# Performance work log

Hardware: AMD Instinct MI355X
Metric: run time of the kernel (lower is better)

## Reference

```python
import jax, jax.numpy as jnp
import numpy as np
from jax import lax

PATCH = 11          # patch_size
DIL = 2             # dilation_patch
PAD = (PATCH // 2) * DIL  # 10
EPS = 1e-5


def setup_inputs() -> dict:
    key = jax.random.key(0)
    k0, k1, kw, kb, kg, kbe = jax.random.split(key, 6)
    B, C, H, W = 8, 128, 192, 192
    x0 = jax.random.normal(k0, (B, C, H, W), dtype=jnp.float32)
    x1 = jax.random.normal(k1, (B, C, H, W), dtype=jnp.float32)
    # Conv2d(121, 8, k=3, s=1, p=1) params + BatchNorm2d(8) affine params
    conv_w = jax.random.normal(kw, (8, 121, 3, 3), dtype=jnp.float32) * 0.05
    conv_b = jax.random.normal(kb, (8,), dtype=jnp.float32) * 0.05
    gamma = jnp.ones((8,), dtype=jnp.float32)
    beta = jnp.zeros((8,), dtype=jnp.float32)
    return {"x0": x0, "x1": x1, "conv_w": conv_w, "conv_b": conv_b,
            "gamma": gamma, "beta": beta}


def _correlation(x0, x1):
    """spatial_correlation_sample(kernel=1, patch=11, stride=1, pad=0, dil_patch=2).
    out[b, pi*11+pj, i, j] = sum_c x0[b,c,i,j] * x1[b,c, i+(pi-5)*2, j+(pj-5)*2]
    (zero-padded outside)."""
    x1p = jnp.pad(x1, ((0, 0), (0, 0), (PAD, PAD), (PAD, PAD)))
    slices = []
    for pi in range(PATCH):       # static 11x11 displacement grid
        for pj in range(PATCH):
            x1s = lax.dynamic_slice(x1p, (0, 0, pi * DIL, pj * DIL), x1.shape)
            slices.append(jnp.einsum('bchw,bchw->bhw', x0, x1s))
    return jnp.stack(slices, axis=1)  # [B, 121, H, W]


def reference(x0, x1, conv_w, conv_b, gamma, beta):
    y = _correlation(x0, x1)  # [B, 121, H, W]
    y = lax.conv_general_dilated(y, conv_w, window_strides=(1, 1),
                                 padding=((1, 1), (1, 1)),
                                 dimension_numbers=('NCHW', 'OIHW', 'NCHW'))
    y = y + conv_b[None, :, None, None]
    # BatchNorm2d in training mode: batch statistics over (B, H, W), biased var
    mean = jnp.mean(y, axis=(0, 2, 3))
    var = jnp.var(y, axis=(0, 2, 3))
    y = (y - mean[None, :, None, None]) * (gamma / jnp.sqrt(var + EPS))[None, :, None, None] \
        + beta[None, :, None, None]
    return jax.nn.relu(y)
```

## Files before the change

kernel.cpp:

```cpp
#include <hip/hip_runtime.h>

#define HH 192
#define WW 192
#define CC 128
#define BB 8
#define HW (HH * WW)
#define OC 8
#define NPIX (BB * HW)
#define YCHUNK (OC * BB * HW)
#define X0ROW 24576
#define X1ROW 28672

typedef __attribute__((ext_vector_type(8))) short bf16x8;
typedef __attribute__((ext_vector_type(4))) float f32x4;

__device__ __forceinline__ unsigned short f2bf(float f) {
    unsigned int u = __float_as_uint(f);
    u += 0x7fffu + ((u >> 16) & 1u);
    return (unsigned short)(u >> 16);
}
__device__ __forceinline__ float bf2f(unsigned short u) {
    return __uint_as_float(((unsigned int)u) << 16);
}

__global__ __launch_bounds__(256) void k_pack(
    const float* __restrict__ x0, const float* __restrict__ x1,
    unsigned short* __restrict__ x0t, unsigned short* __restrict__ x1t)
{
    const int h = blockIdx.x, b = blockIdx.y, t = blockIdx.z;
    const float* src = t ? x1 : x0;
    __shared__ unsigned short lds[WW * 130];

    for (int idx = threadIdx.x; idx < CC * WW; idx += 256) {
        const int w = idx % WW, c = idx / WW;
        lds[w * 130 + c] = f2bf(src[((size_t)(b * CC + c) * HH + h) * WW + w]);
    }
    __syncthreads();

    if (t == 0) {
        unsigned int* dst = (unsigned int*)(x0t + (size_t)(b * HH + h) * X0ROW);
        for (int f2 = threadIdx.x; f2 < X0ROW / 2; f2 += 256) {
            const int e2  = f2 & 3;
            const int pxl = (f2 >> 2) & 15;
            const int kg  = (f2 >> 6) & 3;
            const int q   = (f2 >> 8) & 3;
            const int pu  = f2 >> 10;
            const int ut  = pu % 6, par = pu / 6;
            const int px  = 2 * (16 * ut + pxl) + par;
            const int c   = q * 32 + kg * 8 + e2 * 2;
            const unsigned int lo = lds[px * 130 + c];
            const unsigned int hi = lds[px * 130 + c + 1];
            dst[f2] = lo | (hi << 16);
        }
    } else {
        unsigned int* dst = (unsigned int*)(x1t + (size_t)(b * HH + h) * X1ROW);
        for (int f2 = threadIdx.x; f2 < X1ROW / 2; f2 += 256) {
            const int e2  = f2 & 3;
            const int pxl = (f2 >> 2) & 15;
            const int kg  = (f2 >> 6) & 3;
            const int q   = (f2 >> 8) & 3;
            const int pv  = f2 >> 10;
            const int vt  = pv % 7, par = pv / 7;
            const int v   = 16 * vt - 8 + pxl;
            unsigned int val = 0;
            if (v >= 0 && v < 96) {
                const int px = 2 * v + par;
                const int c  = q * 32 + kg * 8 + e2 * 2;
                val = lds[px * 130 + c] | ((unsigned int)lds[px * 130 + c + 1] << 16);
            }
            dst[f2] = val;
        }
    }
}

__global__ __launch_bounds__(384, 8) void k_corr_mfma_conv(
    const unsigned short* __restrict__ x0t, const unsigned short* __restrict__ x1t,
    const float* __restrict__ cw, const float* __restrict__ cb,
    float* __restrict__ y0, float* __restrict__ y1, float* __restrict__ y2)
{
    const int L = blockIdx.x;
    const int w = (L & 7) * 96 + (L >> 3);
    const int b     = w / 96;
    const int rem   = w % 96;
    const int part  = rem >> 5;
    const int strip = rem & 31;
    const int i0    = strip * 6;
    const int plo   = (11 * part) / 3;
    const int phi   = (11 * (part + 1)) / 3;

    const int tid  = threadIdx.x;
    const int wave = tid >> 6, lane = tid & 63;
    const int ln15 = lane & 15, kg = lane >> 4;
    const int u0   = wave * 16;

    __shared__ unsigned short corr[8][194][11];

    if (tid < 176) {
        const int ir = tid / 22, rr = tid % 22;
        const int pj = rr % 11, jj = (rr < 11) ? 0 : 193;
        corr[ir][jj][pj] = 0;
    }

    float yacc[3][OC];
#pragma unroll
    for (int k = 0; k < 3; ++k)
#pragma unroll
        for (int o = 0; o < OC; ++o) yacc[k][o] = 0.f;

    const int jt  = tid % 192;
    const int irb = tid / 192;

    const unsigned short* x0b = x0t + (size_t)b * HH * X0ROW;
    const unsigned short* x1b = x1t + (size_t)b * HH * X1ROW;

    for (int pi = plo; pi < phi; ++pi) {
        __syncthreads();

        for (int ir = 0; ir < 8; ++ir) {
            const int i = i0 - 1 + ir;
            const int r = i + 2 * pi - 10;
            const bool gv = (i >= 0) && (i < HH) && (r >= 0) && (r < HH);
            const int icl = min(max(i, 0), HH - 1);
            const int rcl = min(max(r, 0), HH - 1);
            const unsigned short* arow = x0b + (size_t)icl * X0ROW + lane * 8;
            const unsigned short* brow = x1b + (size_t)rcl * X1ROW + lane * 8;

#pragma unroll
            for (int par = 0; par < 2; ++par) {
                const unsigned short* pa = arow + (par * 6 + wave) * 2048;
                const bf16x8 a0 = *(const bf16x8*)(pa);
                const bf16x8 a1 = *(const bf16x8*)(pa + 512);
                const bf16x8 a2 = *(const bf16x8*)(pa + 1024);
                const bf16x8 a3 = *(const bf16x8*)(pa + 1536);

#pragma unroll
                for (int vtl = 0; vtl < 2; ++vtl) {
                    const unsigned short* pb =
                        brow + (par * 7 + wave + vtl) * 2048;
                    const bf16x8 b0 = *(const bf16x8*)(pb);
                    const bf16x8 b1 = *(const bf16x8*)(pb + 512);
                    const bf16x8 b2 = *(const bf16x8*)(pb + 1024);
                    const bf16x8 b3 = *(const bf16x8*)(pb + 1536);

                    f32x4 c = {0.f, 0.f, 0.f, 0.f};
                    c = __builtin_amdgcn_mfma_f32_16x16x32_bf16(a0, b0, c, 0, 0, 0);
                    c = __builtin_amdgcn_mfma_f32_16x16x32_bf16(a1, b1, c, 0, 0, 0);
                    c = __builtin_amdgcn_mfma_f32_16x16x32_bf16(a2, b2, c, 0, 0, 0);
                    c = __builtin_amdgcn_mfma_f32_16x16x32_bf16(a3, b3, c, 0, 0, 0);

                    const int v = u0 - 8 + 16 * vtl + ln15;
#pragma unroll
                    for (int rg = 0; rg < 4; ++rg) {
                        const int u  = u0 + kg * 4 + rg;
                        const int pj = v - u + 5;
                        if (pj >= 0 && pj < 11)
                            corr[ir][2 * u + par + 1][pj] = f2bf(gv ? c[rg] : 0.f);
                    }
                }
            }
        }
        __syncthreads();

        for (int ki = 0; ki < 3; ++ki) {
            for (int kj = 0; kj < 3; ++kj) {
                float cv[3][11];
#pragma unroll
                for (int k = 0; k < 3; ++k) {
                    const unsigned short* cp = &corr[irb + 2 * k + ki][jt + kj][0];
#pragma unroll
                    for (int pj = 0; pj < 11; ++pj) cv[k][pj] = bf2f(cp[pj]);
                }
#pragma unroll
                for (int o = 0; o < OC; ++o) {
                    float a0 = yacc[0][o], a1 = yacc[1][o], a2 = yacc[2][o];
#pragma unroll
                    for (int pj = 0; pj < 11; ++pj) {
                        const float wv =
                            cw[o * 1089 + (pi * 11 + pj) * 9 + ki * 3 + kj];
                        a0 = fmaf(wv, cv[0][pj], a0);
                        a1 = fmaf(wv, cv[1][pj], a1);
                        a2 = fmaf(wv, cv[2][pj], a2);
                    }
                    yacc[0][o] = a0; yacc[1][o] = a1; yacc[2][o] = a2;
                }
            }
        }
    }

    float* yp = (part == 0) ? y0 : ((part == 1) ? y1 : y2);
#pragma unroll
    for (int k = 0; k < 3; ++k) {
        const int irow = i0 + irb + 2 * k;
#pragma unroll
        for (int o = 0; o < OC; ++o) {
            float val = yacc[k][o];
            if (part == 0) val += cb[o];
            yp[((size_t)(b * OC + o) * HH + irow) * WW + jt] = val;
        }
    }
}

__global__ __launch_bounds__(256) void k_corr_conv(
    const float* __restrict__ x0, const float* __restrict__ x1,
    const float* __restrict__ cw, const float* __restrict__ cb,
    float* __restrict__ y)
{
    const int b  = blockIdx.z;
    const int i0 = blockIdx.y * 14;
    const int j0 = blockIdx.x * 14;
    const int li = threadIdx.x >> 4;
    const int lj = threadIdx.x & 15;
    const int gi = i0 + li - 1;
    const int gj = j0 + lj - 1;
    const bool valid    = (gi >= 0) & (gi < HH) & (gj >= 0) & (gj < WW);
    const bool interior = (li >= 1) & (li <= 14) & (lj >= 1) & (lj <= 14)
                        & (gi < HH) & (gj < WW);

    __shared__ float corr[16][16][13];

    float yacc[OC];
#pragma unroll
    for (int o = 0; o < OC; ++o) yacc[o] = 0.f;

    const size_t bbase = (size_t)b * CC * HW;
    const float* x0p = x0 + bbase + (size_t)gi * WW + gj;

    for (int pi = 0; pi < 11; ++pi) {
        float acc[11];
#pragma unroll
        for (int k = 0; k < 11; ++k) acc[k] = 0.f;

        const int r = gi + 2 * pi - 10;
        if (valid && r >= 0 && r < HH) {
            const float* p0 = x0p;
            if (gj >= 10 && gj <= WW - 11) {
                const float* p1o = x1 + bbase + (size_t)r * WW + (gj - 10);
#pragma unroll 2
                for (int c = 0; c < CC; ++c) {
                    const float a = *p0;
#pragma unroll
                    for (int k = 0; k < 11; ++k)
                        acc[k] = fmaf(a, p1o[2 * k], acc[k]);
                    p0 += HW; p1o += HW;
                }
            } else {
                const float* p1 = x1 + bbase + (size_t)r * WW;
#pragma unroll 2
                for (int c = 0; c < CC; ++c) {
                    const float a = *p0;
#pragma unroll
                    for (int k = 0; k < 11; ++k) {
                        const int col = gj + 2 * k - 10;
                        const float v = (col >= 0 && col < WW) ? p1[col] : 0.f;
                        acc[k] = fmaf(a, v, acc[k]);
                    }
                    p0 += HW; p1 += HW;
                }
            }
        }

        __syncthreads();
#pragma unroll
        for (int k = 0; k < 11; ++k) corr[li][lj][k] = acc[k];
        __syncthreads();

        if (interior) {
#pragma unroll
            for (int ki = 0; ki < 3; ++ki) {
#pragma unroll
                for (int kj = 0; kj < 3; ++kj) {
                    float cv[11];
#pragma unroll
                    for (int k = 0; k < 11; ++k)
                        cv[k] = corr[li + ki - 1][lj + kj - 1][k];
#pragma unroll
                    for (int o = 0; o < OC; ++o) {
#pragma unroll
                        for (int k = 0; k < 11; ++k) {
                            const float wv =
                                cw[(((o * 121) + pi * 11 + k) * 3 + ki) * 3 + kj];
                            yacc[o] = fmaf(wv, cv[k], yacc[o]);
                        }
                    }
                }
            }
        }
    }

    if (interior) {
#pragma unroll
        for (int o = 0; o < OC; ++o)
            y[(size_t)(b * OC + o) * HW + (size_t)gi * WW + gj] = yacc[o] + cb[o];
    }
}

__global__ __launch_bounds__(256) void k_stats_partial(
    const float* __restrict__ y0, const float* __restrict__ y1,
    const float* __restrict__ y2, int n, float* __restrict__ st)
{
    const int bid = blockIdx.x;
    const int b = bid >> 5, rem = bid & 31;
    const int o = rem >> 2, q = rem & 3;
    const size_t off = (size_t)(b * OC + o) * (HW / 4) + q * (HW / 16);
    const float4* p0 = (const float4*)y0 + off;
    const float4* p1 = (const float4*)y1 + off;
    const float4* p2 = (const float4*)y2 + off;
    float s = 0.f, qq = 0.f;
    for (int t = threadIdx.x; t < HW / 16; t += 256) {
        float4 z = p0[t];
        if (n >= 2) {
            const float4 v = p1[t];
            z.x += v.x; z.y += v.y; z.z += v.z; z.w += v.w;
        }
        if (n >= 3) {
            const float4 v = p2[t];
            z.x += v.x; z.y += v.y; z.z += v.z; z.w += v.w;
        }
        s += z.x + z.y + z.z + z.w;
        qq = fmaf(z.x, z.x, qq); qq = fmaf(z.y, z.y, qq);
        qq = fmaf(z.z, z.z, qq); qq = fmaf(z.w, z.w, qq);
    }
#pragma unroll
    for (int off2 = 32; off2 > 0; off2 >>= 1) {
        s  += __shfl_down(s, off2);
        qq += __shfl_down(qq, off2);
    }
    __shared__ float ss[4], sq[4];
    const int lane = threadIdx.x & 63, wv = threadIdx.x >> 6;
    if (lane == 0) { ss[wv] = s; sq[wv] = qq; }
    __syncthreads();
    if (threadIdx.x == 0) {
        st[bid]       = ss[0] + ss[1] + ss[2] + ss[3];
        st[256 + bid] = sq[0] + sq[1] + sq[2] + sq[3];
    }
}

__global__ void k_stats_final(float* __restrict__ st,
                              const float* __restrict__ gamma,
                              const float* __restrict__ beta)
{
    const int o = threadIdx.x;
    if (o < 8) {
        float S = 0.f, Q = 0.f;
#pragma unroll
        for (int b = 0; b < 8; ++b)
#pragma unroll
            for (int q = 0; q < 4; ++q) {
                S += st[b * 32 + o * 4 + q];
                Q += st[256 + b * 32 + o * 4 + q];
            }
        const float invN = 1.f / (float)NPIX;
        const float mean = S * invN;
        const float var  = Q * invN - mean * mean;
        const float sc   = gamma[o] / sqrtf(var + 1e-5f);
        st[512 + o] = sc;
        st[520 + o] = beta[o] - mean * sc;
    }
}

__global__ __launch_bounds__(256) void k_bn_relu(
    const float* __restrict__ y0, const float* __restrict__ y1,
    const float* __restrict__ y2, int n,
    const float* __restrict__ st, float* __restrict__ out)
{
    const int i = blockIdx.x * 256 + threadIdx.x;
    const int o = (i / (HW / 4)) & 7;
    const float sc = st[512 + o], sh = st[520 + o];
    float4 z = ((const float4*)y0)[i];
    if (n >= 2) {
        const float4 v = ((const float4*)y1)[i];
        z.x += v.x; z.y += v.y; z.z += v.z; z.w += v.w;
    }
    if (n >= 3) {
        const float4 v = ((const float4*)y2)[i];
        z.x += v.x; z.y += v.y; z.z += v.z; z.w += v.w;
    }
    float4 r;
    r.x = fmaxf(fmaf(z.x, sc, sh), 0.f);
    r.y = fmaxf(fmaf(z.y, sc, sh), 0.f);
    r.z = fmaxf(fmaf(z.z, sc, sh), 0.f);
    r.w = fmaxf(fmaf(z.w, sc, sh), 0.f);
    ((float4*)out)[i] = r;
}

extern "C" void kernel_launch(void* const* d_in, const int* in_sizes, int n_in,
                              void* d_out, int out_size, void* d_ws, size_t ws_size,
                              hipStream_t stream)
{
    const float* x0    = (const float*)d_in[0];
    const float* x1    = (const float*)d_in[1];
    const float* cw    = (const float*)d_in[2];
    const float* cb    = (const float*)d_in[3];
    const float* gamma = (const float*)d_in[4];
    const float* beta  = (const float*)d_in[5];
    float* out = (float*)d_out;
    float* st  = (float*)d_ws;

    const size_t x0bytes = (size_t)BB * HH * X0ROW * sizeof(unsigned short);
    const size_t x1bytes = (size_t)BB * HH * X1ROW * sizeof(unsigned short);
    const size_t ybytes  = (size_t)YCHUNK * sizeof(float);

    if (ws_size >= x0bytes + x1bytes + 2 * ybytes) {
        unsigned short* x0t = (unsigned short*)d_ws;
        unsigned short* x1t = (unsigned short*)((char*)d_ws + x0bytes);
        float* y1           = (float*)((char*)d_ws + x0bytes + x1bytes);
        float* y2           = (float*)((char*)d_ws + x0bytes + x1bytes + ybytes);

        k_pack<<<dim3(HH, BB, 2), 256, 0, stream>>>(x0, x1, x0t, x1t);
        k_corr_mfma_conv<<<768, 384, 0, stream>>>(x0t, x1t, cw, cb, out, y1, y2);
        k_stats_partial<<<256, 256, 0, stream>>>(out, y1, y2, 3, st);
        k_stats_final<<<1, 64, 0, stream>>>(st, gamma, beta);
        k_bn_relu<<<(YCHUNK / 4) / 256, 256, 0, stream>>>(out, y1, y2, 3, st, out);
    } else {
        dim3 g1(14, 14, 8);
        k_corr_conv<<<g1, 256, 0, stream>>>(x0, x1, cw, cb, out);
        k_stats_partial<<<256, 256, 0, stream>>>(out, out, out, 1, st);
        k_stats_final<<<1, 64, 0, stream>>>(st, gamma, beta);
        k_bn_relu<<<(YCHUNK / 4) / 256, 256, 0, stream>>>(out, out, out, 1, st, out);
    }
}
```

Baseline: 530.9 us.

## Process two pi displacement rows per sync and split work into two parts

The correlation+conv kernel now splits the 11 vertical displacements across 2 parts instead of 3, giving 512 blocks instead of 768. Within each block it computes two pi rows per iteration into a double-sized LDS correlation buffer. This reuses the x0 fragment loads across both displacements and halves the number of barriers. It also drops one partial-output buffer and the stats/BN pass over it. In exchange, LDS use and register pressure rise, occupancy falls (the launch-bounds min-blocks hint is removed), and fewer blocks may underfill the GPU.

Result: slower. 554.7 us (+4.5%).

```diff
diff --git a/kernel.cpp b/kernel.cpp
--- a/kernel.cpp
+++ b/kernel.cpp
@@ -73,32 +73,33 @@
     }
 }
 
-__global__ __launch_bounds__(384, 8) void k_corr_mfma_conv(
+__global__ __launch_bounds__(384) void k_corr_mfma_conv(
     const unsigned short* __restrict__ x0t, const unsigned short* __restrict__ x1t,
     const float* __restrict__ cw, const float* __restrict__ cb,
-    float* __restrict__ y0, float* __restrict__ y1, float* __restrict__ y2)
+    float* __restrict__ y0, float* __restrict__ y1)
 {
     const int L = blockIdx.x;
-    const int w = (L & 7) * 96 + (L >> 3);
-    const int b     = w / 96;
-    const int rem   = w % 96;
+    const int w = (L & 7) * 64 + (L >> 3);
+    const int b     = w >> 6;
+    const int rem   = w & 63;
     const int part  = rem >> 5;
     const int strip = rem & 31;
     const int i0    = strip * 6;
-    const int plo   = (11 * part) / 3;
-    const int phi   = (11 * (part + 1)) / 3;
+    const int plo   = part ? 6 : 0;
+    const int phi   = part ? 11 : 6;
 
     const int tid  = threadIdx.x;
     const int wave = tid >> 6, lane = tid & 63;
     const int ln15 = lane & 15, kg = lane >> 4;
     const int u0   = wave * 16;
 
-    __shared__ unsigned short corr[8][194][11];
-
-    if (tid < 176) {
-        const int ir = tid / 22, rr = tid % 22;
+    __shared__ unsigned short corr[2][8][194][11];
+
+    if (tid < 352) {
+        const int sl = tid / 176, r2 = tid % 176;
+        const int ir = r2 / 22, rr = r2 % 22;
         const int pj = rr % 11, jj = (rr < 11) ? 0 : 193;
-        corr[ir][jj][pj] = 0;
+        corr[sl][ir][jj][pj] = 0;
     }
 
     float yacc[3][OC];
@@ -113,17 +114,15 @@
     const unsigned short* x0b = x0t + (size_t)b * HH * X0ROW;
     const unsigned short* x1b = x1t + (size_t)b * HH * X1ROW;
 
-    for (int pi = plo; pi < phi; ++pi) {
+    for (int p0 = plo; p0 < phi; p0 += 2) {
+        const int npair = (p0 + 1 < phi) ? 2 : 1;
         __syncthreads();
 
         for (int ir = 0; ir < 8; ++ir) {
-            const int i = i0 - 1 + ir;
-            const int r = i + 2 * pi - 10;
-            const bool gv = (i >= 0) && (i < HH) && (r >= 0) && (r < HH);
+            const int i   = i0 - 1 + ir;
+            const bool iv = (i >= 0) && (i < HH);
             const int icl = min(max(i, 0), HH - 1);
-            const int rcl = min(max(r, 0), HH - 1);
             const unsigned short* arow = x0b + (size_t)icl * X0ROW + lane * 8;
-            const unsigned short* brow = x1b + (size_t)rcl * X1ROW + lane * 8;
 
 #pragma unroll
             for (int par = 0; par < 2; ++par) {
@@ -134,60 +133,80 @@
                 const bf16x8 a3 = *(const bf16x8*)(pa + 1536);
 
 #pragma unroll
-                for (int vtl = 0; vtl < 2; ++vtl) {
-                    const unsigned short* pb =
-                        brow + (par * 7 + wave + vtl) * 2048;
-                    const bf16x8 b0 = *(const bf16x8*)(pb);
-                    const bf16x8 b1 = *(const bf16x8*)(pb + 512);
-                    const bf16x8 b2 = *(const bf16x8*)(pb + 1024);
-                    const bf16x8 b3 = *(const bf16x8*)(pb + 1536);
-
-                    f32x4 c = {0.f, 0.f, 0.f, 0.f};
-                    c = __builtin_amdgcn_mfma_f32_16x16x32_bf16(a0, b0, c, 0, 0, 0);
-                    c = __builtin_amdgcn_mfma_f32_16x16x32_bf16(a1, b1, c, 0, 0, 0);
-                    c = __builtin_amdgcn_mfma_f32_16x16x32_bf16(a2, b2, c, 0, 0, 0);
-                    c = __builtin_amdgcn_mfma_f32_16x16x32_bf16(a3, b3, c, 0, 0, 0);
-
-                    const int v = u0 - 8 + 16 * vtl + ln15;
-#pragma unroll
-                    for (int rg = 0; rg < 4; ++rg) {
-                        const int u  = u0 + kg * 4 + rg;
-                        const int pj = v - u + 5;
-                        if (pj >= 0 && pj < 11)
-                            corr[ir][2 * u + par + 1][pj] = f2bf(gv ? c[rg] : 0.f);
+                for (int p2 = 0; p2 < 2; ++p2) {
+                    if (p2 < npair) {
+                        const int pi = p0 + p2;
+                        const int r  = i + 2 * pi - 10;
+                        const bool gv = iv && (r >= 0) && (r < HH);
+                        const int rcl = min(max(r, 0), HH - 1);
+                        const unsigned short* brow =
+                            x1b + (size_t)rcl * X1ROW + lane * 8;
+
+#pragma unroll
+                        for (int vtl = 0; vtl < 2; ++vtl) {
+                            const unsigned short* pb =
+                                brow + (par * 7 + wave + vtl) * 2048;
+                            const bf16x8 b0 = *(const bf16x8*)(pb);
+                            const bf16x8 b1 = *(const bf16x8*)(pb + 512);
+                            const bf16x8 b2 = *(const bf16x8*)(pb + 1024);
+                            const bf16x8 b3 = *(const bf16x8*)(pb + 1536);
+
+                            f32x4 c = {0.f, 0.f, 0.f, 0.f};
+                            c = __builtin_amdgcn_mfma_f32_16x16x32_bf16(a0, b0, c, 0, 0, 0);
+                            c = __builtin_amdgcn_mfma_f32_16x16x32_bf16(a1, b1, c, 0, 0, 0);
+                            c = __builtin_amdgcn_mfma_f32_16x16x32_bf16(a2, b2, c, 0, 0, 0);
+                            c = __builtin_amdgcn_mfma_f32_16x16x32_bf16(a3, b3, c, 0, 0, 0);
+
+                            const int v = u0 - 8 + 16 * vtl + ln15;
+#pragma unroll
+                            for (int rg = 0; rg < 4; ++rg) {
+                                const int u  = u0 + kg * 4 + rg;
+                                const int pj = v - u + 5;
+                                if (pj >= 0 && pj < 11)
+                                    corr[p2][ir][2 * u + par + 1][pj] =
+                                        f2bf(gv ? c[rg] : 0.f);
+                            }
+                        }
                     }
                 }
             }
         }
         __syncthreads();
 
-        for (int ki = 0; ki < 3; ++ki) {
-            for (int kj = 0; kj < 3; ++kj) {
-                float cv[3][11];
-#pragma unroll
-                for (int k = 0; k < 3; ++k) {
-                    const unsigned short* cp = &corr[irb + 2 * k + ki][jt + kj][0];
-#pragma unroll
-                    for (int pj = 0; pj < 11; ++pj) cv[k][pj] = bf2f(cp[pj]);
+#pragma unroll
+        for (int p2 = 0; p2 < 2; ++p2) {
+            if (p2 < npair) {
+                const int pi = p0 + p2;
+                for (int ki = 0; ki < 3; ++ki) {
+                    for (int kj = 0; kj < 3; ++kj) {
+                        float cv[3][11];
+#pragma unroll
+                        for (int k = 0; k < 3; ++k) {
+                            const unsigned short* cp =
+                                &corr[p2][irb + 2 * k + ki][jt + kj][0];
+#pragma unroll
+                            for (int pj = 0; pj < 11; ++pj) cv[k][pj] = bf2f(cp[pj]);
+                        }
+#pragma unroll
+                        for (int o = 0; o < OC; ++o) {
+                            float a0 = yacc[0][o], a1 = yacc[1][o], a2 = yacc[2][o];
+#pragma unroll
+                            for (int pj = 0; pj < 11; ++pj) {
+                                const float wv =
+                                    cw[o * 1089 + (pi * 11 + pj) * 9 + ki * 3 + kj];
+                                a0 = fmaf(wv, cv[0][pj], a0);
+                                a1 = fmaf(wv, cv[1][pj], a1);
+                                a2 = fmaf(wv, cv[2][pj], a2);
+                            }
+                            yacc[0][o] = a0; yacc[1][o] = a1; yacc[2][o] = a2;
+                        }
+                    }
                 }
-#pragma unroll
-                for (int o = 0; o < OC; ++o) {
-                    float a0 = yacc[0][o], a1 = yacc[1][o], a2 = yacc[2][o];
-#pragma unroll
-                    for (int pj = 0; pj < 11; ++pj) {
-                        const float wv =
-                            cw[o * 1089 + (pi * 11 + pj) * 9 + ki * 3 + kj];
-                        a0 = fmaf(wv, cv[0][pj], a0);
-                        a1 = fmaf(wv, cv[1][pj], a1);
-                        a2 = fmaf(wv, cv[2][pj], a2);
-                    }
-                    yacc[0][o] = a0; yacc[1][o] = a1; yacc[2][o] = a2;
-                }
-            }
-        }
-    }
-
-    float* yp = (part == 0) ? y0 : ((part == 1) ? y1 : y2);
+            }
+        }
+    }
+
+    float* yp = part ? y1 : y0;
 #pragma unroll
     for (int k = 0; k < 3; ++k) {
         const int irow = i0 + irb + 2 * k;
@@ -400,17 +419,16 @@
     const size_t x1bytes = (size_t)BB * HH * X1ROW * sizeof(unsigned short);
     const size_t ybytes  = (size_t)YCHUNK * sizeof(float);
 
-    if (ws_size >= x0bytes + x1bytes + 2 * ybytes) {
+    if (ws_size >= x0bytes + x1bytes + ybytes) {
         unsigned short* x0t = (unsigned short*)d_ws;
         unsigned short* x1t = (unsigned short*)((char*)d_ws + x0bytes);
         float* y1           = (float*)((char*)d_ws + x0bytes + x1bytes);
-        float* y2           = (float*)((char*)d_ws + x0bytes + x1bytes + ybytes);
 
         k_pack<<<dim3(HH, BB, 2), 256, 0, stream>>>(x0, x1, x0t, x1t);
-        k_corr_mfma_conv<<<768, 384, 0, stream>>>(x0t, x1t, cw, cb, out, y1, y2);
-        k_stats_partial<<<256, 256, 0, stream>>>(out, y1, y2, 3, st);
+        k_corr_mfma_conv<<<512, 384, 0, stream>>>(x0t, x1t, cw, cb, out, y1);
+        k_stats_partial<<<256, 256, 0, stream>>>(out, y1, y1, 2, st);
         k_stats_final<<<1, 64, 0, stream>>>(st, gamma, beta);
-        k_bn_relu<<<(YCHUNK / 4) / 256, 256, 0, stream>>>(out, y1, y2, 3, st, out);
+        k_bn_relu<<<(YCHUNK / 4) / 256, 256, 0, stream>>>(out, y1, y1, 2, st, out);
     } else {
         dim3 g1(14, 14, 8);
         k_corr_conv<<<g1, 256, 0, stream>>>(x0, x1, cw, cb, out);
```

## Double-buffer MFMA operand loads in correlation loop and vectorize pack stores

Applied to the files above, without the earlier changes.

The correlation phase now software-pipelines its global loads: operands for the next (row, parity) step are loaded into a second register set while MFMAs run on the current one, so memory latency can hide behind compute. Launch bounds drop from 8 to 4 waves-per-EU minimum to give the extra register buffers room, at the cost of occupancy. The pack kernel also writes 16-byte vectors instead of 4-byte words.

After: 795.9 us. 49.9% more time.

```diff
diff --git a/kernel.cpp b/kernel.cpp
--- a/kernel.cpp
+++ b/kernel.cpp
@@ -38,42 +38,95 @@
     __syncthreads();
 
     if (t == 0) {
-        unsigned int* dst = (unsigned int*)(x0t + (size_t)(b * HH + h) * X0ROW);
-        for (int f2 = threadIdx.x; f2 < X0ROW / 2; f2 += 256) {
-            const int e2  = f2 & 3;
-            const int pxl = (f2 >> 2) & 15;
-            const int kg  = (f2 >> 6) & 3;
-            const int q   = (f2 >> 8) & 3;
-            const int pu  = f2 >> 10;
+        uint4* dst = (uint4*)(x0t + (size_t)(b * HH + h) * X0ROW);
+        for (int f8 = threadIdx.x; f8 < X0ROW / 8; f8 += 256) {
+            const int pxl = f8 & 15;
+            const int kg  = (f8 >> 4) & 3;
+            const int q   = (f8 >> 6) & 3;
+            const int pu  = f8 >> 8;
             const int ut  = pu % 6, par = pu / 6;
             const int px  = 2 * (16 * ut + pxl) + par;
-            const int c   = q * 32 + kg * 8 + e2 * 2;
-            const unsigned int lo = lds[px * 130 + c];
-            const unsigned int hi = lds[px * 130 + c + 1];
-            dst[f2] = lo | (hi << 16);
+            const unsigned short* s0 = &lds[px * 130 + q * 32 + kg * 8];
+            uint4 v;
+            v.x = s0[0] | ((unsigned int)s0[1] << 16);
+            v.y = s0[2] | ((unsigned int)s0[3] << 16);
+            v.z = s0[4] | ((unsigned int)s0[5] << 16);
+            v.w = s0[6] | ((unsigned int)s0[7] << 16);
+            dst[f8] = v;
         }
     } else {
-        unsigned int* dst = (unsigned int*)(x1t + (size_t)(b * HH + h) * X1ROW);
-        for (int f2 = threadIdx.x; f2 < X1ROW / 2; f2 += 256) {
-            const int e2  = f2 & 3;
-            const int pxl = (f2 >> 2) & 15;
-            const int kg  = (f2 >> 6) & 3;
-            const int q   = (f2 >> 8) & 3;
-            const int pv  = f2 >> 10;
+        uint4* dst = (uint4*)(x1t + (size_t)(b * HH + h) * X1ROW);
+        for (int f8 = threadIdx.x; f8 < X1ROW / 8; f8 += 256) {
+            const int pxl = f8 & 15;
+            const int kg  = (f8 >> 4) & 3;
+            const int q   = (f8 >> 6) & 3;
+            const int pv  = f8 >> 8;
             const int vt  = pv % 7, par = pv / 7;
             const int v   = 16 * vt - 8 + pxl;
-            unsigned int val = 0;
+            uint4 val = {0u, 0u, 0u, 0u};
             if (v >= 0 && v < 96) {
                 const int px = 2 * v + par;
-                const int c  = q * 32 + kg * 8 + e2 * 2;
-                val = lds[px * 130 + c] | ((unsigned int)lds[px * 130 + c + 1] << 16);
+                const unsigned short* s0 = &lds[px * 130 + q * 32 + kg * 8];
+                val.x = s0[0] | ((unsigned int)s0[1] << 16);
+                val.y = s0[2] | ((unsigned int)s0[3] << 16);
+                val.z = s0[4] | ((unsigned int)s0[5] << 16);
+                val.w = s0[6] | ((unsigned int)s0[7] << 16);
             }
-            dst[f2] = val;
-        }
-    }
-}
-
-__global__ __launch_bounds__(384, 8) void k_corr_mfma_conv(
+            dst[f8] = val;
+        }
+    }
+}
+
+#define LOAD_STEP(FA, FB, PI, S)                                              \
+  do {                                                                        \
+    const int irL = (S) >> 1, parL = (S) & 1;                                 \
+    const int iL  = i0 - 1 + irL;                                             \
+    const int rL  = iL + 2 * (PI) - 10;                                       \
+    const int icL = min(max(iL, 0), HH - 1);                                  \
+    const int rcL = min(max(rL, 0), HH - 1);                                  \
+    const unsigned short* paL = x0b + (size_t)icL * X0ROW + lane * 8          \
+                              + (parL * 6 + wave) * 2048;                     \
+    FA[0] = *(const bf16x8*)(paL);                                            \
+    FA[1] = *(const bf16x8*)(paL + 512);                                      \
+    FA[2] = *(const bf16x8*)(paL + 1024);                                     \
+    FA[3] = *(const bf16x8*)(paL + 1536);                                     \
+    const unsigned short* pbL = x1b + (size_t)rcL * X1ROW + lane * 8          \
+                              + (parL * 7 + wave) * 2048;                     \
+    FB[0][0] = *(const bf16x8*)(pbL);                                         \
+    FB[0][1] = *(const bf16x8*)(pbL + 512);                                   \
+    FB[0][2] = *(const bf16x8*)(pbL + 1024);                                  \
+    FB[0][3] = *(const bf16x8*)(pbL + 1536);                                  \
+    FB[1][0] = *(const bf16x8*)(pbL + 2048);                                  \
+    FB[1][1] = *(const bf16x8*)(pbL + 2560);                                  \
+    FB[1][2] = *(const bf16x8*)(pbL + 3072);                                  \
+    FB[1][3] = *(const bf16x8*)(pbL + 3584);                                  \
+  } while (0)
+
+#define COMPUTE_STEP(FA, FB, PI, S)                                           \
+  do {                                                                        \
+    const int irC = (S) >> 1, parC = (S) & 1;                                 \
+    const int iC  = i0 - 1 + irC;                                             \
+    const int rC  = iC + 2 * (PI) - 10;                                       \
+    const bool gvC = (iC >= 0) && (iC < HH) && (rC >= 0) && (rC < HH);        \
+    _Pragma("unroll")                                                         \
+    for (int vtl = 0; vtl < 2; ++vtl) {                                       \
+      f32x4 c = {0.f, 0.f, 0.f, 0.f};                                         \
+      c = __builtin_amdgcn_mfma_f32_16x16x32_bf16(FA[0], FB[vtl][0], c,0,0,0);\
+      c = __builtin_amdgcn_mfma_f32_16x16x32_bf16(FA[1], FB[vtl][1], c,0,0,0);\
+      c = __builtin_amdgcn_mfma_f32_16x16x32_bf16(FA[2], FB[vtl][2], c,0,0,0);\
+      c = __builtin_amdgcn_mfma_f32_16x16x32_bf16(FA[3], FB[vtl][3], c,0,0,0);\
+      const int vC = u0 - 8 + 16 * vtl + ln15;                                \
+      _Pragma("unroll")                                                       \
+      for (int rg = 0; rg < 4; ++rg) {                                        \
+        const int uC  = u0 + kg * 4 + rg;                                     \
+        const int pjC = vC - uC + 5;                                          \
+        if (pjC >= 0 && pjC < 11)                                             \
+          corr[irC][2 * uC + parC + 1][pjC] = f2bf(gvC ? c[rg] : 0.f);        \
+      }                                                                       \
+    }                                                                         \
+  } while (0)
+
+__global__ __launch_bounds__(384, 4) void k_corr_mfma_conv(
     const unsigned short* __restrict__ x0t, const unsigned short* __restrict__ x1t,
     const float* __restrict__ cw, const float* __restrict__ cb,
     float* __restrict__ y0, float* __restrict__ y1, float* __restrict__ y2)
@@ -116,48 +169,15 @@
     for (int pi = plo; pi < phi; ++pi) {
         __syncthreads();
 
-        for (int ir = 0; ir < 8; ++ir) {
-            const int i = i0 - 1 + ir;
-            const int r = i + 2 * pi - 10;
-            const bool gv = (i >= 0) && (i < HH) && (r >= 0) && (r < HH);
-            const int icl = min(max(i, 0), HH - 1);
-            const int rcl = min(max(r, 0), HH - 1);
-            const unsigned short* arow = x0b + (size_t)icl * X0ROW + lane * 8;
-            const unsigned short* brow = x1b + (size_t)rcl * X1ROW + lane * 8;
-
-#pragma unroll
-            for (int par = 0; par < 2; ++par) {
-                const unsigned short* pa = arow + (par * 6 + wave) * 2048;
-                const bf16x8 a0 = *(const bf16x8*)(pa);
-                const bf16x8 a1 = *(const bf16x8*)(pa + 512);
-                const bf16x8 a2 = *(const bf16x8*)(pa + 1024);
-                const bf16x8 a3 = *(const bf16x8*)(pa + 1536);
-
-#pragma unroll
-                for (int vtl = 0; vtl < 2; ++vtl) {
-                    const unsigned short* pb =
-                        brow + (par * 7 + wave + vtl) * 2048;
-                    const bf16x8 b0 = *(const bf16x8*)(pb);
-                    const bf16x8 b1 = *(const bf16x8*)(pb + 512);
-                    const bf16x8 b2 = *(const bf16x8*)(pb + 1024);
-                    const bf16x8 b3 = *(const bf16x8*)(pb + 1536);
-
-                    f32x4 c = {0.f, 0.f, 0.f, 0.f};
-                    c = __builtin_amdgcn_mfma_f32_16x16x32_bf16(a0, b0, c, 0, 0, 0);
-                    c = __builtin_amdgcn_mfma_f32_16x16x32_bf16(a1, b1, c, 0, 0, 0);
-                    c = __builtin_amdgcn_mfma_f32_16x16x32_bf16(a2, b2, c, 0, 0, 0);
-                    c = __builtin_amdgcn_mfma_f32_16x16x32_bf16(a3, b3, c, 0, 0, 0);
-
-                    const int v = u0 - 8 + 16 * vtl + ln15;
-#pragma unroll
-                    for (int rg = 0; rg < 4; ++rg) {
-                        const int u  = u0 + kg * 4 + rg;
-                        const int pj = v - u + 5;
-                        if (pj >= 0 && pj < 11)
-                            corr[ir][2 * u + par + 1][pj] = f2bf(gv ? c[rg] : 0.f);
-                    }
-                }
-            }
+        bf16x8 A0[4], A1[4];
+        bf16x8 B0[2][4], B1[2][4];
+        LOAD_STEP(A0, B0, pi, 0);
+#pragma unroll
+        for (int sp = 0; sp < 8; ++sp) {
+            LOAD_STEP(A1, B1, pi, 2 * sp + 1);
+            COMPUTE_STEP(A0, B0, pi, 2 * sp);
+            if (sp < 7) LOAD_STEP(A0, B0, pi, 2 * sp + 2);
+            COMPUTE_STEP(A1, B1, pi, 2 * sp + 1);
         }
         __syncthreads();
 
```

## Stage conv weights in LDS, vectorize corr/pack accesses, rebalance MFMA work

Applied to the files above, without the earlier changes.

Several changes at once. The pack kernel now writes 16-byte stores instead of 4-byte ones. The correlation kernel stages the per-pi conv weights in shared memory and reads them as float4, replacing scalar global loads. The corr tile is padded to 12 entries so each row can be read as bf16x4 vectors. The MFMA phase uses a flat work loop over 96 (row, parity, tile) tasks spread across waves, and the launch-bounds occupancy hint drops from 8 to 6. These aim to cut global load traffic and LDS instruction count in the conv stage, at the cost of extra shared memory and lower occupancy.

Measured after the change: 2.020 ms. 280% more time.

```diff
diff --git a/kernel.cpp b/kernel.cpp
--- a/kernel.cpp
+++ b/kernel.cpp
@@ -12,6 +12,7 @@
 #define X1ROW 28672
 
 typedef __attribute__((ext_vector_type(8))) short bf16x8;
+typedef __attribute__((ext_vector_type(4))) short bf16x4;
 typedef __attribute__((ext_vector_type(4))) float f32x4;
 
 __device__ __forceinline__ unsigned short f2bf(float f) {
@@ -38,42 +39,46 @@
     __syncthreads();
 
     if (t == 0) {
-        unsigned int* dst = (unsigned int*)(x0t + (size_t)(b * HH + h) * X0ROW);
-        for (int f2 = threadIdx.x; f2 < X0ROW / 2; f2 += 256) {
-            const int e2  = f2 & 3;
-            const int pxl = (f2 >> 2) & 15;
-            const int kg  = (f2 >> 6) & 3;
-            const int q   = (f2 >> 8) & 3;
-            const int pu  = f2 >> 10;
+        uint4* dst = (uint4*)(x0t + (size_t)(b * HH + h) * X0ROW);
+        for (int f8 = threadIdx.x; f8 < X0ROW / 8; f8 += 256) {
+            const int pxl = f8 & 15;
+            const int kg  = (f8 >> 4) & 3;
+            const int q   = (f8 >> 6) & 3;
+            const int pu  = f8 >> 8;
             const int ut  = pu % 6, par = pu / 6;
             const int px  = 2 * (16 * ut + pxl) + par;
-            const int c   = q * 32 + kg * 8 + e2 * 2;
-            const unsigned int lo = lds[px * 130 + c];
-            const unsigned int hi = lds[px * 130 + c + 1];
-            dst[f2] = lo | (hi << 16);
+            const unsigned short* s0 = &lds[px * 130 + q * 32 + kg * 8];
+            uint4 v;
+            v.x = s0[0] | ((unsigned int)s0[1] << 16);
+            v.y = s0[2] | ((unsigned int)s0[3] << 16);
+            v.z = s0[4] | ((unsigned int)s0[5] << 16);
+            v.w = s0[6] | ((unsigned int)s0[7] << 16);
+            dst[f8] = v;
         }
     } else {
-        unsigned int* dst = (unsigned int*)(x1t + (size_t)(b * HH + h) * X1ROW);
-        for (int f2 = threadIdx.x; f2 < X1ROW / 2; f2 += 256) {
-            const int e2  = f2 & 3;
-            const int pxl = (f2 >> 2) & 15;
-            const int kg  = (f2 >> 6) & 3;
-            const int q   = (f2 >> 8) & 3;
-            const int pv  = f2 >> 10;
+        uint4* dst = (uint4*)(x1t + (size_t)(b * HH + h) * X1ROW);
+        for (int f8 = threadIdx.x; f8 < X1ROW / 8; f8 += 256) {
+            const int pxl = f8 & 15;
+            const int kg  = (f8 >> 4) & 3;
+            const int q   = (f8 >> 6) & 3;
+            const int pv  = f8 >> 8;
             const int vt  = pv % 7, par = pv / 7;
             const int v   = 16 * vt - 8 + pxl;
-            unsigned int val = 0;
+            uint4 val = {0u, 0u, 0u, 0u};
             if (v >= 0 && v < 96) {
                 const int px = 2 * v + par;
-                const int c  = q * 32 + kg * 8 + e2 * 2;
-                val = lds[px * 130 + c] | ((unsigned int)lds[px * 130 + c + 1] << 16);
-            }
-            dst[f2] = val;
-        }
-    }
-}
-
-__global__ __launch_bounds__(384, 8) void k_corr_mfma_conv(
+                const unsigned short* s0 = &lds[px * 130 + q * 32 + kg * 8];
+                val.x = s0[0] | ((unsigned int)s0[1] << 16);
+                val.y = s0[2] | ((unsigned int)s0[3] << 16);
+                val.z = s0[4] | ((unsigned int)s0[5] << 16);
+                val.w = s0[6] | ((unsigned int)s0[7] << 16);
+            }
+            dst[f8] = val;
+        }
+    }
+}
+
+__global__ __launch_bounds__(384, 6) void k_corr_mfma_conv(
     const unsigned short* __restrict__ x0t, const unsigned short* __restrict__ x1t,
     const float* __restrict__ cw, const float* __restrict__ cb,
     float* __restrict__ y0, float* __restrict__ y1, float* __restrict__ y2)
@@ -93,7 +98,8 @@
     const int ln15 = lane & 15, kg = lane >> 4;
     const int u0   = wave * 16;
 
-    __shared__ unsigned short corr[8][194][11];
+    __shared__ unsigned short corr[8][194][12];
+    __shared__ float wlds[9][8][12];
 
     if (tid < 176) {
         const int ir = tid / 22, rr = tid % 22;
@@ -116,46 +122,53 @@
     for (int pi = plo; pi < phi; ++pi) {
         __syncthreads();
 
-        for (int ir = 0; ir < 8; ++ir) {
-            const int i = i0 - 1 + ir;
-            const int r = i + 2 * pi - 10;
+        for (int idx = tid; idx < 792; idx += 384) {
+            const int o  = idx / 99;
+            const int r2 = idx % 99;
+            const int pj = r2 / 9;
+            const int kk = r2 % 9;
+            wlds[kk][o][pj] = cw[o * 1089 + (pi * 11 + pj) * 9 + kk];
+        }
+
+        for (int g = wave; g < 96; g += 6) {
+            const int ir  = g / 12, rr = g % 12;
+            const int par = rr / 6, ut = rr % 6;
+            const int u0g = ut * 16;
+            const int i   = i0 - 1 + ir;
+            const int r   = i + 2 * pi - 10;
             const bool gv = (i >= 0) && (i < HH) && (r >= 0) && (r < HH);
             const int icl = min(max(i, 0), HH - 1);
             const int rcl = min(max(r, 0), HH - 1);
-            const unsigned short* arow = x0b + (size_t)icl * X0ROW + lane * 8;
-            const unsigned short* brow = x1b + (size_t)rcl * X1ROW + lane * 8;
-
-#pragma unroll
-            for (int par = 0; par < 2; ++par) {
-                const unsigned short* pa = arow + (par * 6 + wave) * 2048;
-                const bf16x8 a0 = *(const bf16x8*)(pa);
-                const bf16x8 a1 = *(const bf16x8*)(pa + 512);
-                const bf16x8 a2 = *(const bf16x8*)(pa + 1024);
-                const bf16x8 a3 = *(const bf16x8*)(pa + 1536);
-
-#pragma unroll
-                for (int vtl = 0; vtl < 2; ++vtl) {
-                    const unsigned short* pb =
-                        brow + (par * 7 + wave + vtl) * 2048;
-                    const bf16x8 b0 = *(const bf16x8*)(pb);
-                    const bf16x8 b1 = *(const bf16x8*)(pb + 512);
-                    const bf16x8 b2 = *(const bf16x8*)(pb + 1024);
-                    const bf16x8 b3 = *(const bf16x8*)(pb + 1536);
-
-                    f32x4 c = {0.f, 0.f, 0.f, 0.f};
-                    c = __builtin_amdgcn_mfma_f32_16x16x32_bf16(a0, b0, c, 0, 0, 0);
-                    c = __builtin_amdgcn_mfma_f32_16x16x32_bf16(a1, b1, c, 0, 0, 0);
-                    c = __builtin_amdgcn_mfma_f32_16x16x32_bf16(a2, b2, c, 0, 0, 0);
-                    c = __builtin_amdgcn_mfma_f32_16x16x32_bf16(a3, b3, c, 0, 0, 0);
-
-                    const int v = u0 - 8 + 16 * vtl + ln15;
-#pragma unroll
-                    for (int rg = 0; rg < 4; ++rg) {
-                        const int u  = u0 + kg * 4 + rg;
-                        const int pj = v - u + 5;
-                        if (pj >= 0 && pj < 11)
-                            corr[ir][2 * u + par + 1][pj] = f2bf(gv ? c[rg] : 0.f);
-                    }
+
+            const unsigned short* pa =
+                x0b + (size_t)icl * X0ROW + (par * 6 + ut) * 2048 + lane * 8;
+            const bf16x8 a0 = *(const bf16x8*)(pa);
+            const bf16x8 a1 = *(const bf16x8*)(pa + 512);
+            const bf16x8 a2 = *(const bf16x8*)(pa + 1024);
+            const bf16x8 a3 = *(const bf16x8*)(pa + 1536);
+
+#pragma unroll
+            for (int vtl = 0; vtl < 2; ++vtl) {
+                const unsigned short* pb =
+                    x1b + (size_t)rcl * X1ROW + (par * 7 + ut + vtl) * 2048 + lane * 8;
+                const bf16x8 b0 = *(const bf16x8*)(pb);
+                const bf16x8 b1 = *(const bf16x8*)(pb + 512);
+                const bf16x8 b2 = *(const bf16x8*)(pb + 1024);
+                const bf16x8 b3 = *(const bf16x8*)(pb + 1536);
+
+                f32x4 c = {0.f, 0.f, 0.f, 0.f};
+                c = __builtin_amdgcn_mfma_f32_16x16x32_bf16(a0, b0, c, 0, 0, 0);
+                c = __builtin_amdgcn_mfma_f32_16x16x32_bf16(a1, b1, c, 0, 0, 0);
+                c = __builtin_amdgcn_mfma_f32_16x16x32_bf16(a2, b2, c, 0, 0, 0);
+                c = __builtin_amdgcn_mfma_f32_16x16x32_bf16(a3, b3, c, 0, 0, 0);
+
+                const int v = u0g - 8 + 16 * vtl + ln15;
+#pragma unroll
+                for (int rg = 0; rg < 4; ++rg) {
+                    const int u  = u0g + kg * 4 + rg;
+                    const int pj = v - u + 5;
+                    if (pj >= 0 && pj < 11)
+                        corr[ir][2 * u + par + 1][pj] = f2bf(gv ? c[rg] : 0.f);
                 }
             }
         }
@@ -163,24 +176,44 @@
 
         for (int ki = 0; ki < 3; ++ki) {
             for (int kj = 0; kj < 3; ++kj) {
+                const int kk = ki * 3 + kj;
                 float cv[3][11];
 #pragma unroll
                 for (int k = 0; k < 3; ++k) {
                     const unsigned short* cp = &corr[irb + 2 * k + ki][jt + kj][0];
-#pragma unroll
-                    for (int pj = 0; pj < 11; ++pj) cv[k][pj] = bf2f(cp[pj]);
+                    const bf16x4 q0 = *(const bf16x4*)(cp);
+                    const bf16x4 q1 = *(const bf16x4*)(cp + 4);
+                    const bf16x4 q2 = *(const bf16x4*)(cp + 8);
+                    cv[k][0] = bf2f((unsigned short)q0[0]);
+                    cv[k][1] = bf2f((unsigned short)q0[1]);
+                    cv[k][2] = bf2f((unsigned short)q0[2]);
+                    cv[k][3] = bf2f((unsigned short)q0[3]);
+                    cv[k][4] = bf2f((unsigned short)q1[0]);
+                    cv[k][5] = bf2f((unsigned short)q1[1]);
+                    cv[k][6] = bf2f((unsigned short)q1[2]);
+                    cv[k][7] = bf2f((unsigned short)q1[3]);
+                    cv[k][8] = bf2f((unsigned short)q2[0]);
+                    cv[k][9] = bf2f((unsigned short)q2[1]);
+                    cv[k][10] = bf2f((unsigned short)q2[2]);
                 }
 #pragma unroll
                 for (int o = 0; o < OC; ++o) {
+                    const float4 wA = *(const float4*)&wlds[kk][o][0];
+                    const float4 wB = *(const float4*)&wlds[kk][o][4];
+                    const float2 wC = *(const float2*)&wlds[kk][o][8];
+                    const float w10 = wlds[kk][o][10];
                     float a0 = yacc[0][o], a1 = yacc[1][o], a2 = yacc[2][o];
-#pragma unroll
-                    for (int pj = 0; pj < 11; ++pj) {
-                        const float wv =
-                            cw[o * 1089 + (pi * 11 + pj) * 9 + ki * 3 + kj];
-                        a0 = fmaf(wv, cv[0][pj], a0);
-                        a1 = fmaf(wv, cv[1][pj], a1);
-                        a2 = fmaf(wv, cv[2][pj], a2);
-                    }
+                    a0 = fmaf(wA.x, cv[0][0], a0); a1 = fmaf(wA.x, cv[1][0], a1); a2 = fmaf(wA.x, cv[2][0], a2);
+                    a0 = fmaf(wA.y, cv[0][1], a0); a1 = fmaf(wA.y, cv[1][1], a1); a2 = fmaf(wA.y, cv[2][1], a2);
+                    a0 = fmaf(wA.z, cv[0][2], a0); a1 = fmaf(wA.z, cv[1][2], a1); a2 = fmaf(wA.z, cv[2][2], a2);
+                    a0 = fmaf(wA.w, cv[0][3], a0); a1 = fmaf(wA.w, cv[1][3], a1); a2 = fmaf(wA.w, cv[2][3], a2);
+                    a0 = fmaf(wB.x, cv[0][4], a0); a1 = fmaf(wB.x, cv[1][4], a1); a2 = fmaf(wB.x, cv[2][4], a2);
+                    a0 = fmaf(wB.y, cv[0][5], a0); a1 = fmaf(wB.y, cv[1][5], a1); a2 = fmaf(wB.y, cv[2][5], a2);
+                    a0 = fmaf(wB.z, cv[0][6], a0); a1 = fmaf(wB.z, cv[1][6], a1); a2 = fmaf(wB.z, cv[2][6], a2);
+                    a0 = fmaf(wB.w, cv[0][7], a0); a1 = fmaf(wB.w, cv[1][7], a1); a2 = fmaf(wB.w, cv[2][7], a2);
+                    a0 = fmaf(wC.x, cv[0][8], a0); a1 = fmaf(wC.x, cv[1][8], a1); a2 = fmaf(wC.x, cv[2][8], a2);
+                    a0 = fmaf(wC.y, cv[0][9], a0); a1 = fmaf(wC.y, cv[1][9], a1); a2 = fmaf(wC.y, cv[2][9], a2);
+                    a0 = fmaf(w10, cv[0][10], a0); a1 = fmaf(w10, cv[1][10], a1); a2 = fmaf(w10, cv[2][10], a2);
                     yacc[0][o] = a0; yacc[1][o] = a1; yacc[2][o] = a2;
                 }
             }
```
